# Kernel tuning notes

Measured on AMD Instinct MI355X. Metric: run time of the kernel, lower is better.

## Reference

```python
import jax, jax.numpy as jnp
import numpy as np

B, I, S, H, O = 128, 64, 2048, 128, 64


def setup_inputs() -> dict:
    key = jax.random.key(0)
    ks = jax.random.split(key, 9)
    sc = 0.1
    return {
        "x": jax.random.normal(ks[0], (B, I, S), dtype=jnp.float32),
        "Wx_out": jax.random.normal(ks[1], (I, 4 * H), dtype=jnp.float32) * sc,
        "Wh_out": jax.random.normal(ks[2], (H, 4 * H), dtype=jnp.float32) * sc,
        "b_out": jnp.zeros((4 * H,), dtype=jnp.float32),
        "Wx_in": jax.random.normal(ks[3], (H, 4 * H), dtype=jnp.float32) * sc,
        "Wh_in": jax.random.normal(ks[4], (H, 4 * H), dtype=jnp.float32) * sc,
        "b_in": jnp.zeros((4 * H,), dtype=jnp.float32),
        "W_lin": jax.random.normal(ks[5], (O, H), dtype=jnp.float32) * 0.01,
        "b_lin": jnp.zeros((O,), dtype=jnp.float32),
    }


def reference(x, Wx_out, Wh_out, b_out, Wx_in, Wh_in, b_in, W_lin, b_lin):
    # x: (B, I, S) -> permute(0,2,1) -> (B, S, I); scan over time axis.
    xs = jnp.transpose(x, (2, 0, 1))  # (S, B, I)
    h0 = jnp.zeros((x.shape[0], Wh_out.shape[0]), dtype=x.dtype)

    def step(carry, xt):
        h, c, cn = carry  # outer hidden, outer cell, inner cell
        gates = xt @ Wx_out + h @ Wh_out + b_out
        i, f, o, g = jnp.split(gates, 4, axis=-1)
        i, f, o = jax.nn.sigmoid(i), jax.nn.sigmoid(f), jax.nn.sigmoid(o)
        g = jnp.tanh(g)
        x_in = i * g          # inner LSTM input
        h_in = f * c          # inner LSTM hidden
        gi = x_in @ Wx_in + h_in @ Wh_in + b_in
        ii, fi, oi, gg = jnp.split(gi, 4, axis=-1)
        cn_new = jax.nn.sigmoid(fi) * cn + jax.nn.sigmoid(ii) * jnp.tanh(gg)
        c_new = jax.nn.sigmoid(oi) * jnp.tanh(cn_new)  # outer cell = inner hidden
        h_new = o * jnp.tanh(c_new)
        return (h_new, c_new, cn_new), h_new

    _, hs = jax.lax.scan(step, (h0, h0, h0), xs)  # hs: (S, B, H)
    hs = jnp.transpose(hs, (1, 0, 2))             # (B, S, H)
    return hs @ W_lin.T + b_lin                   # (B, S, O)
```

## Files before the change

### kernel.cpp

```cpp
#include <hip/hip_runtime.h>
#include <hip/hip_fp16.h>

#define BB 128
#define II 64
#define SS 2048
#define HH 128
#define GG 512
#define OO 64

typedef _Float16 f16x2 __attribute__((ext_vector_type(2)));
union F4H { float4 f4; f16x2 h[4]; };

__device__ __forceinline__ f16x2 pack2(float a, float b) {
    f16x2 r; r.x = (_Float16)a; r.y = (_Float16)b; return r;
}

__device__ __forceinline__ float dot2(f16x2 w, f16x2 v, float c) {
#if __has_builtin(__builtin_amdgcn_fdot2)
    return __builtin_amdgcn_fdot2(w, v, c, false);
#else
    return fmaf((float)w.x, (float)v.x, fmaf((float)w.y, (float)v.y, c));
#endif
}

__device__ __forceinline__ float tanh_f(float v) {
    float a = fabsf(v);
    float e = __expf(-2.0f * a);
    float r = (1.0f - e) * __builtin_amdgcn_rcpf(1.0f + e);
    return v < 0.0f ? -r : r;
}

template<int C>
__device__ __forceinline__ float qb(float v) {
    return __int_as_float(__builtin_amdgcn_mov_dpp(
        __float_as_int(v), 0x55 * C, 0xF, 0xF, true));
}
template<int N>
__device__ __forceinline__ float rolN(float v) {
    return __int_as_float(__builtin_amdgcn_mov_dpp(
        __float_as_int(v), 0x120 + (16 - N), 0xF, 0xF, true));
}

__device__ __forceinline__ void barrier_lds() {
    asm volatile("s_waitcnt lgkmcnt(0)\n\ts_barrier" ::: "memory");
}

template<bool PROJ_IN>
__global__ void __launch_bounds__(512)
__attribute__((amdgpu_waves_per_eu(2)))
nlstm_scan(
    const float* __restrict__ x,
    const float* __restrict__ Wx_out, const float* __restrict__ Wh_out,
    const float* __restrict__ b_out,
    const float* __restrict__ Wx_in, const float* __restrict__ Wh_in,
    const float* __restrict__ b_in,
    const float* __restrict__ W_lin, const float* __restrict__ b_lin,
    float* __restrict__ out, f16x2* __restrict__ hws)
{
    const int b = blockIdx.x;
    const int j = threadIdx.x;
    const int u = j >> 2;
    const int g = j & 3;
    const int jcol = g * HH + u;

    __shared__ __align__(16) float4 wxf[8 * 512];
    __shared__ __align__(16) f16x2 xt[2][16][36];
    __shared__ __align__(16) f16x2 hb[HH / 2];
    __shared__ __align__(16) f16x2 xib[HH / 2];
    __shared__ __align__(16) f16x2 hib[HH / 2];

    f16x2 who[HH / 2];
    f16x2 wxi[HH / 2];
    f16x2 whi[HH / 2];
#pragma unroll
    for (int m = 0; m < HH / 2; ++m)
        who[m] = pack2(Wh_out[(2 * m) * GG + jcol], Wh_out[(2 * m + 1) * GG + jcol]);
#pragma unroll
    for (int m = 0; m < HH / 2; ++m)
        wxi[m] = pack2(Wx_in[(2 * m) * GG + jcol], Wx_in[(2 * m + 1) * GG + jcol]);
#pragma unroll
    for (int m = 0; m < HH / 2; ++m)
        whi[m] = pack2(Wh_in[(2 * m) * GG + jcol], Wh_in[(2 * m + 1) * GG + jcol]);

    const float bo  = b_out[jcol];
    const float bi2 = b_in[jcol];

    const int   pn = j >> 3;
    const int   ps = j & 7;
    float bl = 0.f;
    F4H wl[2];
    if constexpr (PROJ_IN) {
        bl = b_lin[pn];
#pragma unroll
        for (int q = 0; q < 2; ++q) {
            const int c = 2 * ps + q;
#pragma unroll
            for (int r = 0; r < 4; ++r)
                wl[q].h[r] = pack2(W_lin[pn * HH + 8 * c + 2 * r],
                                   W_lin[pn * HH + 8 * c + 2 * r + 1]);
        }
    }

#pragma unroll
    for (int c = 0; c < 8; ++c) {
        F4H w4;
#pragma unroll
        for (int q = 0; q < 4; ++q)
            w4.h[q] = pack2(Wx_out[(8 * c + 2 * q) * GG + jcol],
                            Wx_out[(8 * c + 2 * q + 1) * GG + jcol]);
        wxf[c * 512 + j] = w4.f4;
    }

    const float* xrow = x + (size_t)b * II * SS;
    float* orow = out + (size_t)b * SS * OO;
    f16x2* hrow = hws + (size_t)b * SS * (HH / 2);

    const int xm  = j >> 4;
    const int xtl = j & 15;
    const float* xg0 = xrow + (size_t)(2 * xm) * SS + xtl;
    const float* xg1 = xrow + (size_t)(2 * xm + 1) * SS + xtl;

    xt[0][xtl][xm] = pack2(xg0[0], xg1[0]);
    if (j < HH / 2) hb[j] = pack2(0.f, 0.f);
    __syncthreads();

    float c_reg = 0.f, cn_reg = 0.f;

    const float4* hb4 = (const float4*)hb;
    const float4* xi4 = (const float4*)xib;
    const float4* hi4 = (const float4*)hib;
    const bool isT = (g == 3);

    float pr0 = 0.f, pr1 = 0.f;

#pragma unroll 1
    for (int t = 0; t < SS; ++t) {
        const int stl = t & 15;
        const int tb  = (t >> 4) & 1;

        if (stl == 0) {
            const int Tn = (t + 16 < SS) ? t + 16 : t;
            pr0 = xg0[Tn];
            pr1 = xg1[Tn];
        }

        const float4* xc4 = (const float4*)&xt[tb][stl][0];
        float a0 = 0.f, a1 = 0.f, a2 = 0.f, a3 = 0.f;
#pragma unroll
        for (int c = 0; c < 8; ++c) {
            F4H xu; xu.f4 = xc4[c];
            F4H wu; wu.f4 = wxf[c * 512 + j];
            a0 = dot2(wu.h[0], xu.h[0], a0);
            a1 = dot2(wu.h[1], xu.h[1], a1);
            a2 = dot2(wu.h[2], xu.h[2], a2);
            a3 = dot2(wu.h[3], xu.h[3], a3);
        }
#pragma unroll
        for (int c = 0; c < 16; ++c) {
            F4H hu; hu.f4 = hb4[c];
            a0 = dot2(who[4 * c + 0], hu.h[0], a0);
            a1 = dot2(who[4 * c + 1], hu.h[1], a1);
            a2 = dot2(who[4 * c + 2], hu.h[2], a2);
            a3 = dot2(who[4 * c + 3], hu.h[3], a3);
        }
        float acc = ((a0 + a1) + (a2 + a3)) + bo;

        float ap = isT ? 2.f * acc : acc;
        float s  = __builtin_amdgcn_rcpf(1.f + __expf(-ap));
        float av = isT ? fmaf(2.f, s, -1.f) : s;

        float vi = qb<0>(av), vf = qb<1>(av), vo = qb<2>(av), vg = qb<3>(av);
        float x_in    = vi * vg;
        float h_in    = vf * c_reg;
        float o_outer = vo;

        if constexpr (PROJ_IN) {
            float p0 = 0.f, p1 = 0.f;
            F4H hu0; hu0.f4 = hb4[2 * ps];
            F4H hu1; hu1.f4 = hb4[2 * ps + 1];
            p0 = dot2(wl[0].h[0], hu0.h[0], p0);
            p1 = dot2(wl[0].h[1], hu0.h[1], p1);
            p0 = dot2(wl[0].h[2], hu0.h[2], p0);
            p1 = dot2(wl[0].h[3], hu0.h[3], p1);
            p0 = dot2(wl[1].h[0], hu1.h[0], p0);
            p1 = dot2(wl[1].h[1], hu1.h[1], p1);
            p0 = dot2(wl[1].h[2], hu1.h[2], p0);
            p1 = dot2(wl[1].h[3], hu1.h[3], p1);
            float p = p0 + p1;
            p += rolN<4>(p);
            p += rolN<2>(p);
            p += rolN<1>(p);
            if (ps == 0 && t > 0) orow[(size_t)(t - 1) * OO + pn] = p + bl;
        }

        float xin_n = rolN<4>(x_in);
        float hin_n = rolN<4>(h_in);
        if ((j & 7) == 0) {
            xib[u >> 1] = pack2(x_in, xin_n);
            hib[u >> 1] = pack2(h_in, hin_n);
        }
        barrier_lds();

        float b0 = 0.f, b1 = 0.f, b2 = 0.f, b3 = 0.f;
#pragma unroll
        for (int c = 0; c < 16; ++c) {
            F4H xu; xu.f4 = xi4[c];
            b0 = dot2(wxi[4 * c + 0], xu.h[0], b0);
            b1 = dot2(wxi[4 * c + 1], xu.h[1], b1);
            b2 = dot2(wxi[4 * c + 2], xu.h[2], b2);
            b3 = dot2(wxi[4 * c + 3], xu.h[3], b3);
        }
#pragma unroll
        for (int c = 0; c < 16; ++c) {
            F4H hu; hu.f4 = hi4[c];
            b0 = dot2(whi[4 * c + 0], hu.h[0], b0);
            b1 = dot2(whi[4 * c + 1], hu.h[1], b1);
            b2 = dot2(whi[4 * c + 2], hu.h[2], b2);
            b3 = dot2(whi[4 * c + 3], hu.h[3], b3);
        }
        float acc2 = ((b0 + b1) + (b2 + b3)) + bi2;

        float ap2 = isT ? 2.f * acc2 : acc2;
        float s2  = __builtin_amdgcn_rcpf(1.f + __expf(-ap2));
        float av2 = isT ? fmaf(2.f, s2, -1.f) : s2;

        float ii = qb<0>(av2), fi = qb<1>(av2), oi = qb<2>(av2), gg = qb<3>(av2);
        float cn_new = fmaf(fi, cn_reg, ii * gg);
        cn_reg = cn_new;
        float c_new = oi * tanh_f(cn_new);
        c_reg = c_new;
        float h_new = o_outer * tanh_f(c_new);

        float hn_n = rolN<4>(h_new);
        if ((j & 7) == 0) {
            f16x2 hp = pack2(h_new, hn_n);
            hb[u >> 1] = hp;
            if constexpr (!PROJ_IN)
                hrow[(size_t)t * (HH / 2) + (j >> 3)] = hp;
        }
        if (stl == 0) xt[tb ^ 1][xtl][xm] = pack2(pr0, pr1);
        barrier_lds();
    }

    if constexpr (PROJ_IN) {
        float p0 = 0.f, p1 = 0.f;
        F4H hu0; hu0.f4 = hb4[2 * ps];
        F4H hu1; hu1.f4 = hb4[2 * ps + 1];
        p0 = dot2(wl[0].h[0], hu0.h[0], p0);
        p1 = dot2(wl[0].h[1], hu0.h[1], p1);
        p0 = dot2(wl[0].h[2], hu0.h[2], p0);
        p1 = dot2(wl[0].h[3], hu0.h[3], p1);
        p0 = dot2(wl[1].h[0], hu1.h[0], p0);
        p1 = dot2(wl[1].h[1], hu1.h[1], p1);
        p0 = dot2(wl[1].h[2], hu1.h[2], p0);
        p1 = dot2(wl[1].h[3], hu1.h[3], p1);
        float p = p0 + p1;
        p += rolN<4>(p);
        p += rolN<2>(p);
        p += rolN<1>(p);
        if (ps == 0) orow[(size_t)(SS - 1) * OO + pn] = p + bl;
    }
}

__global__ void __launch_bounds__(256)
nlstm_proj(const f16x2* __restrict__ hws, const float* __restrict__ W_lin,
           const float* __restrict__ b_lin, float* __restrict__ out)
{
    const int n  = threadIdx.x & 63;
    const int rg = threadIdx.x >> 6;

    f16x2 wn[HH / 2];
#pragma unroll
    for (int k = 0; k < HH / 2; ++k)
        wn[k] = pack2(W_lin[n * HH + 2 * k], W_lin[n * HH + 2 * k + 1]);
    const float bl = b_lin[n];

    const size_t r0 = (size_t)blockIdx.x * 512 + (size_t)rg * 128;
#pragma unroll 1
    for (int rr = 0; rr < 128; ++rr) {
        const size_t r = r0 + rr;
        const float4* hr = (const float4*)(hws + r * (HH / 2));
        float p0 = 0.f, p1 = 0.f, p2 = 0.f, p3 = 0.f;
#pragma unroll
        for (int c = 0; c < 16; ++c) {
            F4H hu; hu.f4 = hr[c];
            p0 = dot2(wn[4 * c + 0], hu.h[0], p0);
            p1 = dot2(wn[4 * c + 1], hu.h[1], p1);
            p2 = dot2(wn[4 * c + 2], hu.h[2], p2);
            p3 = dot2(wn[4 * c + 3], hu.h[3], p3);
        }
        out[r * OO + n] = ((p0 + p1) + (p2 + p3)) + bl;
    }
}

extern "C" void kernel_launch(void* const* d_in, const int* in_sizes, int n_in,
                              void* d_out, int out_size, void* d_ws, size_t ws_size,
                              hipStream_t stream) {
    (void)in_sizes; (void)n_in; (void)out_size;
    const float* x      = (const float*)d_in[0];
    const float* Wx_out = (const float*)d_in[1];
    const float* Wh_out = (const float*)d_in[2];
    const float* b_out  = (const float*)d_in[3];
    const float* Wx_in  = (const float*)d_in[4];
    const float* Wh_in  = (const float*)d_in[5];
    const float* b_in   = (const float*)d_in[6];
    const float* W_lin  = (const float*)d_in[7];
    const float* b_lin  = (const float*)d_in[8];
    float* out = (float*)d_out;

    const size_t h_bytes = (size_t)BB * SS * (HH / 2) * sizeof(f16x2);
    if (d_ws != nullptr && ws_size >= h_bytes) {
        f16x2* hws = (f16x2*)d_ws;
        nlstm_scan<false><<<dim3(BB), dim3(512), 0, stream>>>(
            x, Wx_out, Wh_out, b_out, Wx_in, Wh_in, b_in, W_lin, b_lin,
            out, hws);
        nlstm_proj<<<dim3(512), dim3(256), 0, stream>>>(hws, W_lin, b_lin, out);
    } else {
        nlstm_scan<true><<<dim3(BB), dim3(512), 0, stream>>>(
            x, Wx_out, Wh_out, b_out, Wx_in, Wh_in, b_in, W_lin, b_lin,
            out, (f16x2*)nullptr);
    }
}
```

Measured before the change: 4.103 ms.

## Precompute input gate projection in a parallel kernel before the recurrent scan

Adds a separate fully parallel kernel that computes x_t @ Wx_out + b_out for all timesteps into workspace (fp32, or fp16 when workspace is smaller). The scan kernel then reads one precomputed gate value per thread per step, prefetched one step ahead, instead of doing the Wx_out dot products and x staging inside the serial loop. This shortens the per-step critical path of the recurrence and frees LDS. In exchange it writes and reads a large B*S*512 intermediate through HBM and needs more workspace; the per-step global load latency has to be hidden by the prefetch.

```diff
diff --git a/kernel.cpp b/kernel.cpp
--- a/kernel.cpp
+++ b/kernel.cpp
@@ -45,7 +45,57 @@
     asm volatile("s_waitcnt lgkmcnt(0)\n\ts_barrier" ::: "memory");
 }
 
-template<bool PROJ_IN>
+template<bool F32>
+__global__ void __launch_bounds__(512)
+nlstm_gatex(const float* __restrict__ x, const float* __restrict__ Wx_out,
+            const float* __restrict__ b_out, void* __restrict__ gx)
+{
+    const int bb = blockIdx.x >> 4;
+    const int tc = blockIdx.x & 15;
+    const int j  = threadIdx.x;
+    const int u = j >> 2, g = j & 3;
+    const int jcol = g * HH + u;
+
+    __shared__ __align__(16) f16x2 xs[128][36];
+
+    f16x2 wxo[II / 2];
+#pragma unroll
+    for (int m = 0; m < II / 2; ++m)
+        wxo[m] = pack2(Wx_out[(2 * m) * GG + jcol],
+                       Wx_out[(2 * m + 1) * GG + jcol]);
+    const float bo = b_out[jcol];
+
+    const float* xrow = x + (size_t)bb * II * SS;
+    const int T0 = tc * 128;
+#pragma unroll
+    for (int r = 0; r < 8; ++r) {
+        const int idx = r * 512 + j;
+        const int m = idx >> 7, tt = idx & 127;
+        xs[tt][m] = pack2(xrow[(size_t)(2 * m) * SS + T0 + tt],
+                          xrow[(size_t)(2 * m + 1) * SS + T0 + tt]);
+    }
+    __syncthreads();
+
+#pragma unroll 1
+    for (int tt = 0; tt < 128; ++tt) {
+        const float4* xc4 = (const float4*)&xs[tt][0];
+        float a0 = bo, a1 = 0.f, a2 = 0.f, a3 = 0.f;
+#pragma unroll
+        for (int c = 0; c < 8; ++c) {
+            F4H xu; xu.f4 = xc4[c];
+            a0 = dot2(wxo[4 * c + 0], xu.h[0], a0);
+            a1 = dot2(wxo[4 * c + 1], xu.h[1], a1);
+            a2 = dot2(wxo[4 * c + 2], xu.h[2], a2);
+            a3 = dot2(wxo[4 * c + 3], xu.h[3], a3);
+        }
+        const float v = (a0 + a1) + (a2 + a3);
+        const size_t off = ((size_t)bb * SS + T0 + tt) * GG + j;
+        if constexpr (F32) ((float*)gx)[off] = v;
+        else               ((_Float16*)gx)[off] = (_Float16)v;
+    }
+}
+
+template<int GX, bool PROJ_IN>
 __global__ void __launch_bounds__(512)
 __attribute__((amdgpu_waves_per_eu(2)))
 nlstm_scan(
@@ -55,7 +105,8 @@
     const float* __restrict__ Wx_in, const float* __restrict__ Wh_in,
     const float* __restrict__ b_in,
     const float* __restrict__ W_lin, const float* __restrict__ b_lin,
-    float* __restrict__ out, f16x2* __restrict__ hws)
+    float* __restrict__ out, f16x2* __restrict__ hws,
+    const void* __restrict__ gxv)
 {
     const int b = blockIdx.x;
     const int j = threadIdx.x;
@@ -63,8 +114,8 @@
     const int g = j & 3;
     const int jcol = g * HH + u;
 
-    __shared__ __align__(16) float4 wxf[8 * 512];
-    __shared__ __align__(16) f16x2 xt[2][16][36];
+    __shared__ __align__(16) float4 wxf[GX == 0 ? 8 * 512 : 1];
+    __shared__ __align__(16) f16x2 xt[GX == 0 ? 2 : 1][16][36];
     __shared__ __align__(16) f16x2 hb[HH / 2];
     __shared__ __align__(16) f16x2 xib[HH / 2];
     __shared__ __align__(16) f16x2 hib[HH / 2];
@@ -82,7 +133,7 @@
     for (int m = 0; m < HH / 2; ++m)
         whi[m] = pack2(Wh_in[(2 * m) * GG + jcol], Wh_in[(2 * m + 1) * GG + jcol]);
 
-    const float bo  = b_out[jcol];
+    const float bo  = (GX == 0) ? b_out[j >> 0 ? jcol : jcol] : 0.f;
     const float bi2 = b_in[jcol];
 
     const int   pn = j >> 3;
@@ -101,14 +152,16 @@
         }
     }
 
-#pragma unroll
-    for (int c = 0; c < 8; ++c) {
-        F4H w4;
-#pragma unroll
-        for (int q = 0; q < 4; ++q)
-            w4.h[q] = pack2(Wx_out[(8 * c + 2 * q) * GG + jcol],
-                            Wx_out[(8 * c + 2 * q + 1) * GG + jcol]);
-        wxf[c * 512 + j] = w4.f4;
+    if constexpr (GX == 0) {
+#pragma unroll
+        for (int c = 0; c < 8; ++c) {
+            F4H w4;
+#pragma unroll
+            for (int q = 0; q < 4; ++q)
+                w4.h[q] = pack2(Wx_out[(8 * c + 2 * q) * GG + jcol],
+                                Wx_out[(8 * c + 2 * q + 1) * GG + jcol]);
+            wxf[c * 512 + j] = w4.f4;
+        }
     }
 
     const float* xrow = x + (size_t)b * II * SS;
@@ -120,7 +173,15 @@
     const float* xg0 = xrow + (size_t)(2 * xm) * SS + xtl;
     const float* xg1 = xrow + (size_t)(2 * xm + 1) * SS + xtl;
 
-    xt[0][xtl][xm] = pack2(xg0[0], xg1[0]);
+    const size_t gxbase = (size_t)b * SS * GG + j;
+    const float*    gx32 = (const float*)gxv;
+    const _Float16* gx16 = (const _Float16*)gxv;
+    float gx_cur = 0.f;
+    if constexpr (GX == 2) gx_cur = gx32[gxbase];
+    else if constexpr (GX == 1) gx_cur = (float)gx16[gxbase];
+
+    if constexpr (GX == 0)
+        xt[0][xtl][xm] = pack2(xg0[0], xg1[0]);
     if (j < HH / 2) hb[j] = pack2(0.f, 0.f);
     __syncthreads();
 
@@ -138,22 +199,32 @@
         const int stl = t & 15;
         const int tb  = (t >> 4) & 1;
 
-        if (stl == 0) {
+        float gx_nxt = 0.f;
+        if constexpr (GX != 0) {
+            const int tn = (t + 1 < SS) ? t + 1 : t;
+            if constexpr (GX == 2) gx_nxt = gx32[gxbase + (size_t)tn * GG];
+            else                   gx_nxt = (float)gx16[gxbase + (size_t)tn * GG];
+        } else if (stl == 0) {
             const int Tn = (t + 16 < SS) ? t + 16 : t;
             pr0 = xg0[Tn];
             pr1 = xg1[Tn];
         }
 
-        const float4* xc4 = (const float4*)&xt[tb][stl][0];
-        float a0 = 0.f, a1 = 0.f, a2 = 0.f, a3 = 0.f;
-#pragma unroll
-        for (int c = 0; c < 8; ++c) {
-            F4H xu; xu.f4 = xc4[c];
-            F4H wu; wu.f4 = wxf[c * 512 + j];
-            a0 = dot2(wu.h[0], xu.h[0], a0);
-            a1 = dot2(wu.h[1], xu.h[1], a1);
-            a2 = dot2(wu.h[2], xu.h[2], a2);
-            a3 = dot2(wu.h[3], xu.h[3], a3);
+        float a0, a1 = 0.f, a2 = 0.f, a3 = 0.f;
+        if constexpr (GX != 0) {
+            a0 = gx_cur;
+        } else {
+            a0 = bo;
+            const float4* xc4 = (const float4*)&xt[tb][stl][0];
+#pragma unroll
+            for (int c = 0; c < 8; ++c) {
+                F4H xu; xu.f4 = xc4[c];
+                F4H wu; wu.f4 = wxf[c * 512 + j];
+                a0 = dot2(wu.h[0], xu.h[0], a0);
+                a1 = dot2(wu.h[1], xu.h[1], a1);
+                a2 = dot2(wu.h[2], xu.h[2], a2);
+                a3 = dot2(wu.h[3], xu.h[3], a3);
+            }
         }
 #pragma unroll
         for (int c = 0; c < 16; ++c) {
@@ -163,7 +234,7 @@
             a2 = dot2(who[4 * c + 2], hu.h[2], a2);
             a3 = dot2(who[4 * c + 3], hu.h[3], a3);
         }
-        float acc = ((a0 + a1) + (a2 + a3)) + bo;
+        float acc = (a0 + a1) + (a2 + a3);
 
         float ap = isT ? 2.f * acc : acc;
         float s  = __builtin_amdgcn_rcpf(1.f + __expf(-ap));
@@ -238,7 +309,9 @@
             if constexpr (!PROJ_IN)
                 hrow[(size_t)t * (HH / 2) + (j >> 3)] = hp;
         }
-        if (stl == 0) xt[tb ^ 1][xtl][xm] = pack2(pr0, pr1);
+        if constexpr (GX == 0)
+            if (stl == 0) xt[tb ^ 1][xtl][xm] = pack2(pr0, pr1);
+        if constexpr (GX != 0) gx_cur = gx_nxt;
         barrier_lds();
     }
 
@@ -308,16 +381,38 @@
     const float* b_lin  = (const float*)d_in[8];
     float* out = (float*)d_out;
 
-    const size_t h_bytes = (size_t)BB * SS * (HH / 2) * sizeof(f16x2);
-    if (d_ws != nullptr && ws_size >= h_bytes) {
+    const size_t h_bytes  = (size_t)BB * SS * (HH / 2) * sizeof(f16x2);
+    const size_t gx_elems = (size_t)BB * SS * GG;
+    const size_t gx32_b   = gx_elems * 4;
+    const size_t gx16_b   = gx_elems * 2;
+
+    if (d_ws != nullptr && ws_size >= h_bytes + gx32_b) {
         f16x2* hws = (f16x2*)d_ws;
-        nlstm_scan<false><<<dim3(BB), dim3(512), 0, stream>>>(
+        void* gx = (void*)((char*)d_ws + h_bytes);
+        nlstm_gatex<true><<<dim3(BB * 16), dim3(512), 0, stream>>>(
+            x, Wx_out, b_out, gx);
+        nlstm_scan<2, false><<<dim3(BB), dim3(512), 0, stream>>>(
             x, Wx_out, Wh_out, b_out, Wx_in, Wh_in, b_in, W_lin, b_lin,
-            out, hws);
+            out, hws, gx);
+        nlstm_proj<<<dim3(512), dim3(256), 0, stream>>>(hws, W_lin, b_lin, out);
+    } else if (d_ws != nullptr && ws_size >= h_bytes + gx16_b) {
+        f16x2* hws = (f16x2*)d_ws;
+        void* gx = (void*)((char*)d_ws + h_bytes);
+        nlstm_gatex<false><<<dim3(BB * 16), dim3(512), 0, stream>>>(
+            x, Wx_out, b_out, gx);
+        nlstm_scan<1, false><<<dim3(BB), dim3(512), 0, stream>>>(
+            x, Wx_out, Wh_out, b_out, Wx_in, Wh_in, b_in, W_lin, b_lin,
+            out, hws, gx);
+        nlstm_proj<<<dim3(512), dim3(256), 0, stream>>>(hws, W_lin, b_lin, out);
+    } else if (d_ws != nullptr && ws_size >= h_bytes) {
+        f16x2* hws = (f16x2*)d_ws;
+        nlstm_scan<0, false><<<dim3(BB), dim3(512), 0, stream>>>(
+            x, Wx_out, Wh_out, b_out, Wx_in, Wh_in, b_in, W_lin, b_lin,
+            out, hws, nullptr);
         nlstm_proj<<<dim3(512), dim3(256), 0, stream>>>(hws, W_lin, b_lin, out);
     } else {
-        nlstm_scan<true><<<dim3(BB), dim3(512), 0, stream>>>(
+        nlstm_scan<0, true><<<dim3(BB), dim3(512), 0, stream>>>(
             x, Wx_out, Wh_out, b_out, Wx_in, Wh_in, b_in, W_lin, b_lin,
-            out, (f16x2*)nullptr);
-    }
-}
+            out, (f16x2*)nullptr, nullptr);
+    }
+}
```

Measured after the change: 4.062 ms. About the same (-1.0%).

## Precompute input gate projections in a parallel kernel before the recurrent scan

Applied to the files above, without the earlier changes.

Moves the x@Wx_out + b_out product out of the sequential scan into a separate, fully parallel nlstm_gatex kernel that writes fp32 gate preactivations to workspace. The scan then streams one precomputed value per thread per step, prefetched a step ahead, instead of doing 32 dot2s and LDS tile staging on the critical path. It can run in time segments, carrying h/c/cn state through workspace when space is short. The cost is extra global traffic (BB*SS*512 floats), extra launches, and a global load per step inside the latency-bound recurrence.

```diff
diff --git a/kernel.cpp b/kernel.cpp
--- a/kernel.cpp
+++ b/kernel.cpp
@@ -45,17 +45,67 @@
     asm volatile("s_waitcnt lgkmcnt(0)\n\ts_barrier" ::: "memory");
 }
 
+__global__ void __launch_bounds__(512)
+nlstm_gatex(const float* __restrict__ x, const float* __restrict__ Wx_out,
+            const float* __restrict__ b_out, float* __restrict__ gx,
+            int t0, int nchunk)
+{
+    const int bb  = blockIdx.x / nchunk;
+    const int tcw = blockIdx.x % nchunk;
+    const int j   = threadIdx.x;
+    const int u = j >> 2, g = j & 3;
+    const int jcol = g * HH + u;
+
+    __shared__ __align__(16) f16x2 xs[128][36];
+
+    f16x2 wxo[II / 2];
+#pragma unroll
+    for (int m = 0; m < II / 2; ++m)
+        wxo[m] = pack2(Wx_out[(2 * m) * GG + jcol],
+                       Wx_out[(2 * m + 1) * GG + jcol]);
+    const float bo = b_out[jcol];
+
+    const float* xrow = x + (size_t)bb * II * SS;
+    const int T0 = t0 + tcw * 128;
+#pragma unroll
+    for (int r = 0; r < 8; ++r) {
+        const int idx = r * 512 + j;
+        const int m = idx >> 7, tt = idx & 127;
+        xs[tt][m] = pack2(xrow[(size_t)(2 * m) * SS + T0 + tt],
+                          xrow[(size_t)(2 * m + 1) * SS + T0 + tt]);
+    }
+    __syncthreads();
+
+#pragma unroll 1
+    for (int tt = 0; tt < 128; ++tt) {
+        const float4* xc4 = (const float4*)&xs[tt][0];
+        float a0 = bo, a1 = 0.f, a2 = 0.f, a3 = 0.f;
+#pragma unroll
+        for (int c = 0; c < 8; ++c) {
+            F4H xu; xu.f4 = xc4[c];
+            a0 = dot2(wxo[4 * c + 0], xu.h[0], a0);
+            a1 = dot2(wxo[4 * c + 1], xu.h[1], a1);
+            a2 = dot2(wxo[4 * c + 2], xu.h[2], a2);
+            a3 = dot2(wxo[4 * c + 3], xu.h[3], a3);
+        }
+        const float v = (a0 + a1) + (a2 + a3);
+        const size_t tl = (size_t)tcw * 128 + tt;
+        gx[((size_t)bb * nchunk * 128 + tl) * GG + j] = v;
+    }
+}
+
 template<bool PROJ_IN>
 __global__ void __launch_bounds__(512)
 __attribute__((amdgpu_waves_per_eu(2)))
-nlstm_scan(
-    const float* __restrict__ x,
-    const float* __restrict__ Wx_out, const float* __restrict__ Wh_out,
-    const float* __restrict__ b_out,
+nlstm_scan_seg(
+    const float* __restrict__ Wh_out,
     const float* __restrict__ Wx_in, const float* __restrict__ Wh_in,
     const float* __restrict__ b_in,
     const float* __restrict__ W_lin, const float* __restrict__ b_lin,
-    float* __restrict__ out, f16x2* __restrict__ hws)
+    const float* __restrict__ gx, float* __restrict__ out,
+    f16x2* __restrict__ hws, f16x2* __restrict__ hst,
+    float* __restrict__ cst, float* __restrict__ cnst,
+    int t0, int t1, int Tc)
 {
     const int b = blockIdx.x;
     const int j = threadIdx.x;
@@ -63,8 +113,6 @@
     const int g = j & 3;
     const int jcol = g * HH + u;
 
-    __shared__ __align__(16) float4 wxf[8 * 512];
-    __shared__ __align__(16) f16x2 xt[2][16][36];
     __shared__ __align__(16) f16x2 hb[HH / 2];
     __shared__ __align__(16) f16x2 xib[HH / 2];
     __shared__ __align__(16) f16x2 hib[HH / 2];
@@ -82,7 +130,6 @@
     for (int m = 0; m < HH / 2; ++m)
         whi[m] = pack2(Wh_in[(2 * m) * GG + jcol], Wh_in[(2 * m + 1) * GG + jcol]);
 
-    const float bo  = b_out[jcol];
     const float bi2 = b_in[jcol];
 
     const int   pn = j >> 3;
@@ -101,60 +148,36 @@
         }
     }
 
-#pragma unroll
-    for (int c = 0; c < 8; ++c) {
-        F4H w4;
-#pragma unroll
-        for (int q = 0; q < 4; ++q)
-            w4.h[q] = pack2(Wx_out[(8 * c + 2 * q) * GG + jcol],
-                            Wx_out[(8 * c + 2 * q + 1) * GG + jcol]);
-        wxf[c * 512 + j] = w4.f4;
-    }
-
-    const float* xrow = x + (size_t)b * II * SS;
     float* orow = out + (size_t)b * SS * OO;
-    f16x2* hrow = hws + (size_t)b * SS * (HH / 2);
-
-    const int xm  = j >> 4;
-    const int xtl = j & 15;
-    const float* xg0 = xrow + (size_t)(2 * xm) * SS + xtl;
-    const float* xg1 = xrow + (size_t)(2 * xm + 1) * SS + xtl;
-
-    xt[0][xtl][xm] = pack2(xg0[0], xg1[0]);
-    if (j < HH / 2) hb[j] = pack2(0.f, 0.f);
+    f16x2* hrow = (PROJ_IN ? (f16x2*)nullptr : hws + (size_t)b * SS * (HH / 2));
+    const float* gxrow = gx + (size_t)b * Tc * GG;
+
+    float c_reg, cn_reg;
+    if (t0 == 0) {
+        if (j < HH / 2) hb[j] = pack2(0.f, 0.f);
+        c_reg = 0.f; cn_reg = 0.f;
+    } else {
+        if (j < HH / 2) hb[j] = hst[b * (HH / 2) + j];
+        c_reg  = cst[b * HH + u];
+        cn_reg = cnst[b * HH + u];
+    }
     __syncthreads();
-
-    float c_reg = 0.f, cn_reg = 0.f;
 
     const float4* hb4 = (const float4*)hb;
     const float4* xi4 = (const float4*)xib;
     const float4* hi4 = (const float4*)hib;
     const bool isT = (g == 3);
 
-    float pr0 = 0.f, pr1 = 0.f;
+    float gx_cur = gxrow[j];
 
 #pragma unroll 1
-    for (int t = 0; t < SS; ++t) {
-        const int stl = t & 15;
-        const int tb  = (t >> 4) & 1;
-
-        if (stl == 0) {
-            const int Tn = (t + 16 < SS) ? t + 16 : t;
-            pr0 = xg0[Tn];
-            pr1 = xg1[Tn];
-        }
-
-        const float4* xc4 = (const float4*)&xt[tb][stl][0];
-        float a0 = 0.f, a1 = 0.f, a2 = 0.f, a3 = 0.f;
-#pragma unroll
-        for (int c = 0; c < 8; ++c) {
-            F4H xu; xu.f4 = xc4[c];
-            F4H wu; wu.f4 = wxf[c * 512 + j];
-            a0 = dot2(wu.h[0], xu.h[0], a0);
-            a1 = dot2(wu.h[1], xu.h[1], a1);
-            a2 = dot2(wu.h[2], xu.h[2], a2);
-            a3 = dot2(wu.h[3], xu.h[3], a3);
-        }
+    for (int t = t0; t < t1; ++t) {
+        const int tl = t - t0;
+
+        const int tln = (tl + 1 < Tc) ? tl + 1 : tl;
+        const float gx_nxt = gxrow[(size_t)tln * GG + j];
+
+        float a0 = gx_cur, a1 = 0.f, a2 = 0.f, a3 = 0.f;
 #pragma unroll
         for (int c = 0; c < 16; ++c) {
             F4H hu; hu.f4 = hb4[c];
@@ -163,7 +186,7 @@
             a2 = dot2(who[4 * c + 2], hu.h[2], a2);
             a3 = dot2(who[4 * c + 3], hu.h[3], a3);
         }
-        float acc = ((a0 + a1) + (a2 + a3)) + bo;
+        float acc = (a0 + a1) + (a2 + a3);
 
         float ap = isT ? 2.f * acc : acc;
         float s  = __builtin_amdgcn_rcpf(1.f + __expf(-ap));
@@ -238,11 +261,203 @@
             if constexpr (!PROJ_IN)
                 hrow[(size_t)t * (HH / 2) + (j >> 3)] = hp;
         }
+        gx_cur = gx_nxt;
+        barrier_lds();
+    }
+
+    if (j < HH / 2) hst[b * (HH / 2) + j] = hb[j];
+    if (g == 0) { cst[b * HH + u] = c_reg; cnst[b * HH + u] = cn_reg; }
+
+    if constexpr (PROJ_IN) {
+        if (t1 == SS) {
+            float p0 = 0.f, p1 = 0.f;
+            F4H hu0; hu0.f4 = hb4[2 * ps];
+            F4H hu1; hu1.f4 = hb4[2 * ps + 1];
+            p0 = dot2(wl[0].h[0], hu0.h[0], p0);
+            p1 = dot2(wl[0].h[1], hu0.h[1], p1);
+            p0 = dot2(wl[0].h[2], hu0.h[2], p0);
+            p1 = dot2(wl[0].h[3], hu0.h[3], p1);
+            p0 = dot2(wl[1].h[0], hu1.h[0], p0);
+            p1 = dot2(wl[1].h[1], hu1.h[1], p1);
+            p0 = dot2(wl[1].h[2], hu1.h[2], p0);
+            p1 = dot2(wl[1].h[3], hu1.h[3], p1);
+            float p = p0 + p1;
+            p += rolN<4>(p);
+            p += rolN<2>(p);
+            p += rolN<1>(p);
+            if (ps == 0) orow[(size_t)(SS - 1) * OO + pn] = p + bl;
+        }
+    }
+}
+
+__global__ void __launch_bounds__(512)
+__attribute__((amdgpu_waves_per_eu(2)))
+nlstm_fused(
+    const float* __restrict__ x,
+    const float* __restrict__ Wx_out, const float* __restrict__ Wh_out,
+    const float* __restrict__ b_out,
+    const float* __restrict__ Wx_in, const float* __restrict__ Wh_in,
+    const float* __restrict__ b_in,
+    const float* __restrict__ W_lin, const float* __restrict__ b_lin,
+    float* __restrict__ out)
+{
+    const int b = blockIdx.x;
+    const int j = threadIdx.x;
+    const int u = j >> 2, g = j & 3;
+    const int jcol = g * HH + u;
+
+    __shared__ __align__(16) float4 wxf[8 * 512];
+    __shared__ __align__(16) f16x2 xt[2][16][36];
+    __shared__ __align__(16) f16x2 hb[HH / 2];
+    __shared__ __align__(16) f16x2 xib[HH / 2];
+    __shared__ __align__(16) f16x2 hib[HH / 2];
+
+    f16x2 who[HH / 2], wxi[HH / 2], whi[HH / 2];
+#pragma unroll
+    for (int m = 0; m < HH / 2; ++m)
+        who[m] = pack2(Wh_out[(2 * m) * GG + jcol], Wh_out[(2 * m + 1) * GG + jcol]);
+#pragma unroll
+    for (int m = 0; m < HH / 2; ++m)
+        wxi[m] = pack2(Wx_in[(2 * m) * GG + jcol], Wx_in[(2 * m + 1) * GG + jcol]);
+#pragma unroll
+    for (int m = 0; m < HH / 2; ++m)
+        whi[m] = pack2(Wh_in[(2 * m) * GG + jcol], Wh_in[(2 * m + 1) * GG + jcol]);
+
+    const float bo = b_out[jcol];
+    const float bi2 = b_in[jcol];
+    const int pn = j >> 3, ps = j & 7;
+    const float bl = b_lin[pn];
+    F4H wl[2];
+#pragma unroll
+    for (int q = 0; q < 2; ++q) {
+        const int c = 2 * ps + q;
+#pragma unroll
+        for (int r = 0; r < 4; ++r)
+            wl[q].h[r] = pack2(W_lin[pn * HH + 8 * c + 2 * r],
+                               W_lin[pn * HH + 8 * c + 2 * r + 1]);
+    }
+#pragma unroll
+    for (int c = 0; c < 8; ++c) {
+        F4H w4;
+#pragma unroll
+        for (int q = 0; q < 4; ++q)
+            w4.h[q] = pack2(Wx_out[(8 * c + 2 * q) * GG + jcol],
+                            Wx_out[(8 * c + 2 * q + 1) * GG + jcol]);
+        wxf[c * 512 + j] = w4.f4;
+    }
+
+    const float* xrow = x + (size_t)b * II * SS;
+    float* orow = out + (size_t)b * SS * OO;
+    const int xm = j >> 4, xtl = j & 15;
+    const float* xg0 = xrow + (size_t)(2 * xm) * SS + xtl;
+    const float* xg1 = xrow + (size_t)(2 * xm + 1) * SS + xtl;
+
+    xt[0][xtl][xm] = pack2(xg0[0], xg1[0]);
+    if (j < HH / 2) hb[j] = pack2(0.f, 0.f);
+    __syncthreads();
+
+    float c_reg = 0.f, cn_reg = 0.f;
+    const float4* hb4 = (const float4*)hb;
+    const float4* xi4 = (const float4*)xib;
+    const float4* hi4 = (const float4*)hib;
+    const bool isT = (g == 3);
+    float pr0 = 0.f, pr1 = 0.f;
+
+#pragma unroll 1
+    for (int t = 0; t < SS; ++t) {
+        const int stl = t & 15;
+        const int tb = (t >> 4) & 1;
+        if (stl == 0) {
+            const int Tn = (t + 16 < SS) ? t + 16 : t;
+            pr0 = xg0[Tn];
+            pr1 = xg1[Tn];
+        }
+        const float4* xc4 = (const float4*)&xt[tb][stl][0];
+        float a0 = bo, a1 = 0.f, a2 = 0.f, a3 = 0.f;
+#pragma unroll
+        for (int c = 0; c < 8; ++c) {
+            F4H xu; xu.f4 = xc4[c];
+            F4H wu; wu.f4 = wxf[c * 512 + j];
+            a0 = dot2(wu.h[0], xu.h[0], a0);
+            a1 = dot2(wu.h[1], xu.h[1], a1);
+            a2 = dot2(wu.h[2], xu.h[2], a2);
+            a3 = dot2(wu.h[3], xu.h[3], a3);
+        }
+#pragma unroll
+        for (int c = 0; c < 16; ++c) {
+            F4H hu; hu.f4 = hb4[c];
+            a0 = dot2(who[4 * c + 0], hu.h[0], a0);
+            a1 = dot2(who[4 * c + 1], hu.h[1], a1);
+            a2 = dot2(who[4 * c + 2], hu.h[2], a2);
+            a3 = dot2(who[4 * c + 3], hu.h[3], a3);
+        }
+        float acc = (a0 + a1) + (a2 + a3);
+        float ap = isT ? 2.f * acc : acc;
+        float s = __builtin_amdgcn_rcpf(1.f + __expf(-ap));
+        float av = isT ? fmaf(2.f, s, -1.f) : s;
+        float vi = qb<0>(av), vf = qb<1>(av), vo = qb<2>(av), vg = qb<3>(av);
+        float x_in = vi * vg, h_in = vf * c_reg, o_outer = vo;
+
+        float p0 = 0.f, p1 = 0.f;
+        {
+            F4H hu0; hu0.f4 = hb4[2 * ps];
+            F4H hu1; hu1.f4 = hb4[2 * ps + 1];
+            p0 = dot2(wl[0].h[0], hu0.h[0], p0);
+            p1 = dot2(wl[0].h[1], hu0.h[1], p1);
+            p0 = dot2(wl[0].h[2], hu0.h[2], p0);
+            p1 = dot2(wl[0].h[3], hu0.h[3], p1);
+            p0 = dot2(wl[1].h[0], hu1.h[0], p0);
+            p1 = dot2(wl[1].h[1], hu1.h[1], p1);
+            p0 = dot2(wl[1].h[2], hu1.h[2], p0);
+            p1 = dot2(wl[1].h[3], hu1.h[3], p1);
+        }
+        float p = p0 + p1;
+        p += rolN<4>(p);
+        p += rolN<2>(p);
+        p += rolN<1>(p);
+        if (ps == 0 && t > 0) orow[(size_t)(t - 1) * OO + pn] = p + bl;
+
+        float xin_n = rolN<4>(x_in);
+        float hin_n = rolN<4>(h_in);
+        if ((j & 7) == 0) {
+            xib[u >> 1] = pack2(x_in, xin_n);
+            hib[u >> 1] = pack2(h_in, hin_n);
+        }
+        barrier_lds();
+
+        float b0 = 0.f, b1 = 0.f, b2 = 0.f, b3 = 0.f;
+#pragma unroll
+        for (int c = 0; c < 16; ++c) {
+            F4H xu; xu.f4 = xi4[c];
+            b0 = dot2(wxi[4 * c + 0], xu.h[0], b0);
+            b1 = dot2(wxi[4 * c + 1], xu.h[1], b1);
+            b2 = dot2(wxi[4 * c + 2], xu.h[2], b2);
+            b3 = dot2(wxi[4 * c + 3], xu.h[3], b3);
+        }
+#pragma unroll
+        for (int c = 0; c < 16; ++c) {
+            F4H hu; hu.f4 = hi4[c];
+            b0 = dot2(whi[4 * c + 0], hu.h[0], b0);
+            b1 = dot2(whi[4 * c + 1], hu.h[1], b1);
+            b2 = dot2(whi[4 * c + 2], hu.h[2], b2);
+            b3 = dot2(whi[4 * c + 3], hu.h[3], b3);
+        }
+        float acc2 = ((b0 + b1) + (b2 + b3)) + bi2;
+        float ap2 = isT ? 2.f * acc2 : acc2;
+        float s2 = __builtin_amdgcn_rcpf(1.f + __expf(-ap2));
+        float av2 = isT ? fmaf(2.f, s2, -1.f) : s2;
+        float ii = qb<0>(av2), fi = qb<1>(av2), oi = qb<2>(av2), gg = qb<3>(av2);
+        float cn_new = fmaf(fi, cn_reg, ii * gg);
+        cn_reg = cn_new;
+        float c_new = oi * tanh_f(cn_new);
+        c_reg = c_new;
+        float h_new = o_outer * tanh_f(c_new);
+        float hn_n = rolN<4>(h_new);
+        if ((j & 7) == 0) hb[u >> 1] = pack2(h_new, hn_n);
         if (stl == 0) xt[tb ^ 1][xtl][xm] = pack2(pr0, pr1);
         barrier_lds();
     }
-
-    if constexpr (PROJ_IN) {
+    {
         float p0 = 0.f, p1 = 0.f;
         F4H hu0; hu0.f4 = hb4[2 * ps];
         F4H hu1; hu1.f4 = hb4[2 * ps + 1];
@@ -308,16 +523,50 @@
     const float* b_lin  = (const float*)d_in[8];
     float* out = (float*)d_out;
 
-    const size_t h_bytes = (size_t)BB * SS * (HH / 2) * sizeof(f16x2);
-    if (d_ws != nullptr && ws_size >= h_bytes) {
-        f16x2* hws = (f16x2*)d_ws;
-        nlstm_scan<false><<<dim3(BB), dim3(512), 0, stream>>>(
-            x, Wx_out, Wh_out, b_out, Wx_in, Wh_in, b_in, W_lin, b_lin,
-            out, hws);
-        nlstm_proj<<<dim3(512), dim3(256), 0, stream>>>(hws, W_lin, b_lin, out);
+    const size_t hws_b = (size_t)BB * SS * (HH / 2) * sizeof(f16x2);
+    const size_t hst_b = (size_t)BB * (HH / 2) * sizeof(f16x2);
+    const size_t cst_b = (size_t)BB * HH * sizeof(float);
+    const int tcs[5] = {2048, 1024, 512, 256, 128};
+
+    int Tc = 0;
+    bool proj_out = false;
+    if (d_ws != nullptr) {
+        for (int i = 0; i < 5 && Tc == 0; ++i) {
+            const size_t gxb = (size_t)BB * tcs[i] * GG * sizeof(float);
+            if (ws_size >= hws_b + hst_b + 2 * cst_b + gxb) { Tc = tcs[i]; proj_out = true; }
+        }
+        for (int i = 0; i < 5 && Tc == 0; ++i) {
+            const size_t gxb = (size_t)BB * tcs[i] * GG * sizeof(float);
+            if (ws_size >= hst_b + 2 * cst_b + gxb) Tc = tcs[i];
+        }
+    }
+
+    if (Tc != 0) {
+        char* p = (char*)d_ws;
+        f16x2* hws = nullptr;
+        if (proj_out) { hws = (f16x2*)p; p += hws_b; }
+        f16x2* hst = (f16x2*)p; p += hst_b;
+        float* cst  = (float*)p; p += cst_b;
+        float* cnst = (float*)p; p += cst_b;
+        float* gx   = (float*)p;
+        const int nchunk = Tc / 128;
+
+        for (int t0 = 0; t0 < SS; t0 += Tc) {
+            nlstm_gatex<<<dim3(BB * nchunk), dim3(512), 0, stream>>>(
+                x, Wx_out, b_out, gx, t0, nchunk);
+            if (proj_out)
+                nlstm_scan_seg<false><<<dim3(BB), dim3(512), 0, stream>>>(
+                    Wh_out, Wx_in, Wh_in, b_in, W_lin, b_lin, gx, out,
+                    hws, hst, cst, cnst, t0, t0 + Tc, Tc);
+            else
+                nlstm_scan_seg<true><<<dim3(BB), dim3(512), 0, stream>>>(
+                    Wh_out, Wx_in, Wh_in, b_in, W_lin, b_lin, gx, out,
+                    nullptr, hst, cst, cnst, t0, t0 + Tc, Tc);
+        }
+        if (proj_out)
+            nlstm_proj<<<dim3(512), dim3(256), 0, stream>>>(hws, W_lin, b_lin, out);
     } else {
-        nlstm_scan<true><<<dim3(BB), dim3(512), 0, stream>>>(
-            x, Wx_out, Wh_out, b_out, Wx_in, Wh_in, b_in, W_lin, b_lin,
-            out, (f16x2*)nullptr);
-    }
-}
+        nlstm_fused<<<dim3(BB), dim3(512), 0, stream>>>(
+            x, Wx_out, Wh_out, b_out, Wx_in, Wh_in, b_in, W_lin, b_lin, out);
+    }
+}
```

Measured after the change: 3.841 ms. 1.07x faster.
